# Optimization experiments

Measured on AMD Instinct MI355X. Metric: run time of the kernel, lower is better.

The kernel has to match this reference:

```python
import jax, jax.numpy as jnp
import numpy as np

B, T, C = 4, 2048, 2048
H, HKV = 16, 4
D = C // H            # 128
G = H // HKV          # 4 query heads per kv head
ROPE_THETA = 10000.0


def _rope_tables(seq_len, head_dim, theta):
    inv = 1.0 / (theta ** (np.arange(0, head_dim, 2, dtype=np.float32) / head_dim))
    t = np.arange(seq_len, dtype=np.float32)
    f = np.outer(t, inv)  # (T, D/2)
    return jnp.asarray(np.cos(f)), jnp.asarray(np.sin(f))


def setup_inputs() -> dict:
    key = jax.random.key(0)
    ks = jax.random.split(key, 5)
    x = jax.random.normal(ks[0], (B, T, C), dtype=jnp.float32)
    W_q = jax.random.normal(ks[1], (H * D, C), dtype=jnp.float32) * 0.02
    W_k = jax.random.normal(ks[2], (HKV * D, C), dtype=jnp.float32) * 0.02
    W_v = jax.random.normal(ks[3], (HKV * D, C), dtype=jnp.float32) * 0.02
    W_o = jax.random.normal(ks[4], (C, C), dtype=jnp.float32) * 0.02
    cos, sin = _rope_tables(T, D, ROPE_THETA)
    return {"x": x, "W_q": W_q, "W_k": W_k, "W_v": W_v, "W_o": W_o,
            "cos": cos, "sin": sin}


def _apply_rope(xh, cos, sin):
    # xh: (B, h, T, D); cos/sin: (T, D/2)
    x0 = xh[..., 0::2]
    x1 = xh[..., 1::2]
    c = cos[None, None, :, :]
    s = sin[None, None, :, :]
    o0 = x0 * c - x1 * s
    o1 = x0 * s + x1 * c
    return jnp.stack([o0, o1], axis=-1).reshape(xh.shape)


def reference(x, W_q, W_k, W_v, W_o, cos, sin):
    b, t, c = x.shape
    q = (x @ W_q.T).reshape(b, t, H, D).transpose(0, 2, 1, 3)      # (B,H,T,D)
    k = (x @ W_k.T).reshape(b, t, HKV, D).transpose(0, 2, 1, 3)    # (B,HKV,T,D)
    v = (x @ W_v.T).reshape(b, t, HKV, D).transpose(0, 2, 1, 3)
    q = _apply_rope(q, cos[:t], sin[:t])
    k = _apply_rope(k, cos[:t], sin[:t])
    # GQA via reshape instead of repeat_interleave (same head ordering:
    # q head index h = kv*G + g).
    qg = q.reshape(b, HKV, G, t, D)
    scores = jnp.einsum('bkgtd,bksd->bkgts', qg, k) / jnp.sqrt(jnp.float32(D))
    causal = jnp.tril(jnp.ones((t, t), dtype=bool))
    scores = jnp.where(causal[None, None, None, :, :], scores, -jnp.inf)
    attn = jax.nn.softmax(scores, axis=-1)
    out = jnp.einsum('bkgts,bksd->bkgtd', attn, v)                 # (B,HKV,G,T,D)
    out = out.reshape(b, H, t, D).transpose(0, 2, 1, 3).reshape(b, t, c)
    return out @ W_o.T
```

## Files before the change

### kernel.cpp

```cpp
#include <hip/hip_runtime.h>
#include <cmath>

typedef __attribute__((ext_vector_type(8))) short bf16x8;
typedef __attribute__((ext_vector_type(4))) float f32x4;
typedef unsigned short u16;

__device__ __forceinline__ u16 f2bf(float f) {
  union { float f; unsigned u; } x; x.f = f;
  return (u16)((x.u + 0x7FFFu + ((x.u >> 16) & 1u)) >> 16);
}

__device__ __forceinline__ void gload_lds16(const void* g, void* l) {
  __builtin_amdgcn_global_load_lds((const __attribute__((address_space(1))) unsigned*)g,
                                   (__attribute__((address_space(3))) unsigned*)l,
                                   16, 0, 0);
}

__global__ __launch_bounds__(256) void cast_bf16_kernel(const float* __restrict__ in,
                                                        u16* __restrict__ out, long n) {
  long i = (long)blockIdx.x * blockDim.x + threadIdx.x;
  long stride = (long)gridDim.x * blockDim.x;
  for (long j = i * 4; j < n; j += stride * 4) {
    float4 v = *(const float4*)(in + j);
    ushort4 o;
    o.x = f2bf(v.x); o.y = f2bf(v.y); o.z = f2bf(v.z); o.w = f2bf(v.w);
    *(ushort4*)(out + j) = o;
  }
}

template <int EPI>
__global__ __launch_bounds__(512, 2) void gemm_bt256(const u16* __restrict__ A,
                                                     const u16* __restrict__ B,
                                                     void* __restrict__ outp,
                                                     int M, int N, int K,
                                                     const float* __restrict__ cosp,
                                                     const float* __restrict__ sinp,
                                                     float scale) {
  __shared__ u16 lds[65536];
  const int tid = threadIdx.x;
  const int lane = tid & 63;
  const int l16 = lane & 15, lhi = lane >> 4;
  const int w = tid >> 6;
  const int wr = w >> 2, wc = w & 3;
  const int m0 = blockIdx.y * 256;
  const int n0 = blockIdx.x * 256;

  f32x4 acc[8][4];
#pragma unroll
  for (int i = 0; i < 8; ++i)
#pragma unroll
    for (int j = 0; j < 4; ++j) acc[i][j] = (f32x4)0.0f;

  const int NT = K >> 6;

  auto stage = [&](int t, int buf) {
    const int k0 = t << 6;
    u16* Ad = lds + buf * 32768;
    u16* Bd = Ad + 16384;
#pragma unroll
    for (int j = 0; j < 4; ++j) {
      int c = tid + j * 512;
      int row = c >> 3;
      int sboff = ((c & 7) * 16) ^ ((row & 7) << 4);
      gload_lds16(A + (size_t)(m0 + row) * K + k0 + (sboff >> 1), Ad + (size_t)c * 8);
    }
#pragma unroll
    for (int j = 0; j < 4; ++j) {
      int c = tid + j * 512;
      int row = c >> 3;
      int sboff = ((c & 7) * 16) ^ ((row & 7) << 4);
      gload_lds16(B + (size_t)(n0 + row) * K + k0 + (sboff >> 1), Bd + (size_t)c * 8);
    }
  };

  stage(0, 0);
  stage(1, 1);

  for (int t = 0; t < NT; ++t) {
    const int cur = t & 1;
    if (t + 1 < NT) { asm volatile("s_waitcnt vmcnt(8)" ::: "memory"); }
    else            { asm volatile("s_waitcnt vmcnt(0)" ::: "memory"); }
    __builtin_amdgcn_s_barrier();
    const char* Ab = (const char*)(lds + cur * 32768);
    const char* Bb = (const char*)(lds + cur * 32768 + 16384);
#pragma unroll
    for (int qm = 0; qm < 2; ++qm)
#pragma unroll
      for (int qn = 0; qn < 2; ++qn) {
        bf16x8 af[4][2], bfr[2][2];
#pragma unroll
        for (int mi = 0; mi < 4; ++mi) {
          int ra = wr * 128 + qm * 64 + mi * 16 + l16;
#pragma unroll
          for (int kk = 0; kk < 2; ++kk)
            af[mi][kk] = *(const bf16x8*)(Ab + ra * 128 + ((kk * 64 + lhi * 16) ^ ((ra & 7) << 4)));
        }
#pragma unroll
        for (int ni = 0; ni < 2; ++ni) {
          int rb = wc * 64 + qn * 32 + ni * 16 + l16;
#pragma unroll
          for (int kk = 0; kk < 2; ++kk)
            bfr[ni][kk] = *(const bf16x8*)(Bb + rb * 128 + ((kk * 64 + lhi * 16) ^ ((rb & 7) << 4)));
        }
        __builtin_amdgcn_s_setprio(1);
#pragma unroll
        for (int kk = 0; kk < 2; ++kk)
#pragma unroll
          for (int mi = 0; mi < 4; ++mi)
#pragma unroll
            for (int ni = 0; ni < 2; ++ni)
              acc[qm * 4 + mi][qn * 2 + ni] = __builtin_amdgcn_mfma_f32_16x16x32_bf16(
                  af[mi][kk], bfr[ni][kk], acc[qm * 4 + mi][qn * 2 + ni], 0, 0, 0);
        __builtin_amdgcn_s_setprio(0);
      }
    asm volatile("s_waitcnt lgkmcnt(0)" ::: "memory");
    __builtin_amdgcn_s_barrier();
    if (t + 2 < NT) stage(t + 2, cur);
  }

  if (EPI == 2) {
    float* o = (float*)outp;
#pragma unroll
    for (int mi8 = 0; mi8 < 8; ++mi8)
#pragma unroll
      for (int r = 0; r < 4; ++r) {
        int row = m0 + wr * 128 + mi8 * 16 + lhi * 4 + r;
#pragma unroll
        for (int nj = 0; nj < 4; ++nj) {
          int col = n0 + wc * 64 + nj * 16 + l16;
          o[(size_t)row * N + col] = acc[mi8][nj][r];
        }
      }
  } else {
    u16* o = (u16*)outp;
    const int nheads = N >> 7;
#pragma unroll
    for (int mi8 = 0; mi8 < 8; ++mi8)
#pragma unroll
      for (int r = 0; r < 4; ++r) {
        int row = m0 + wr * 128 + mi8 * 16 + lhi * 4 + r;
        int b = row >> 11;
        int tt = row & 2047;
#pragma unroll
        for (int nj = 0; nj < 4; ++nj) {
          int col = n0 + wc * 64 + nj * 16 + l16;
          int hh = col >> 7, dd = col & 127;
          float v = acc[mi8][nj][r];
          float p = __shfl_xor(v, 1);
          float c = cosp[tt * 64 + (dd >> 1)];
          float s = sinp[tt * 64 + (dd >> 1)];
          v = (lane & 1) ? fmaf(p, s, v * c) : fmaf(v, c, -p * s);
          v *= scale;
          o[((size_t)(b * nheads + hh) * 2048 + tt) * 128 + dd] = f2bf(v);
        }
      }
  }
}

template <int EPI>
__global__ __launch_bounds__(256) void gemm_bt(const u16* __restrict__ A,
                                               const u16* __restrict__ B,
                                               void* __restrict__ outp,
                                               u16* __restrict__ vtp,
                                               int M, int N, int K,
                                               const float* __restrict__ cosp,
                                               const float* __restrict__ sinp,
                                               float scale) {
  __shared__ u16 As[128 * 64];
  __shared__ u16 Bs[128 * 64];
  const int tid = threadIdx.x;
  const int lane = tid & 63;
  const int l16 = lane & 15, lhi = lane >> 4;
  const int w = tid >> 6;
  const int wr = w >> 1, wc = w & 1;
  const int m0 = blockIdx.y * 128;
  const int n0 = blockIdx.x * 128;
  const int wbase = tid - lane;

  f32x4 acc[4][4];
#pragma unroll
  for (int i = 0; i < 4; ++i)
#pragma unroll
    for (int j = 0; j < 4; ++j) acc[i][j] = (f32x4)0.0f;

  for (int k0 = 0; k0 < K; k0 += 64) {
    __syncthreads();
#pragma unroll
    for (int j = 0; j < 4; ++j) {
      int c = tid + j * 256;
      gload_lds16(A + (size_t)(m0 + (c >> 3)) * K + k0 + (c & 7) * 8,
                  As + (size_t)(wbase + j * 256) * 8);
    }
#pragma unroll
    for (int j = 0; j < 4; ++j) {
      int c = tid + j * 256;
      gload_lds16(B + (size_t)(n0 + (c >> 3)) * K + k0 + (c & 7) * 8,
                  Bs + (size_t)(wbase + j * 256) * 8);
    }
    __syncthreads();
#pragma unroll
    for (int kk = 0; kk < 64; kk += 32) {
      bf16x8 af[4], bfr[4];
#pragma unroll
      for (int mi = 0; mi < 4; ++mi)
        af[mi] = *(const bf16x8*)&As[(wr * 64 + mi * 16 + l16) * 64 + kk + lhi * 8];
#pragma unroll
      for (int ni = 0; ni < 4; ++ni)
        bfr[ni] = *(const bf16x8*)&Bs[(wc * 64 + ni * 16 + l16) * 64 + kk + lhi * 8];
#pragma unroll
      for (int mi = 0; mi < 4; ++mi)
#pragma unroll
        for (int ni = 0; ni < 4; ++ni)
          acc[mi][ni] = __builtin_amdgcn_mfma_f32_16x16x32_bf16(af[mi], bfr[ni], acc[mi][ni], 0, 0, 0);
    }
  }

  {
    const int bx = blockIdx.x;
    if (bx < 4) {
      u16* o = (u16*)outp;
#pragma unroll
      for (int mi = 0; mi < 4; ++mi)
#pragma unroll
        for (int r = 0; r < 4; ++r) {
          int row = m0 + wr * 64 + mi * 16 + lhi * 4 + r;
          int b = row >> 11;
          int t = row & 2047;
          size_t base = ((size_t)(b * 4 + bx) * 2048 + t) * 128;
#pragma unroll
          for (int ni = 0; ni < 4; ++ni) {
            int d = wc * 64 + ni * 16 + l16;
            float v = acc[mi][ni][r];
            float p = __shfl_xor(v, 1);
            float c = cosp[t * 64 + (d >> 1)];
            float s = sinp[t * 64 + (d >> 1)];
            v = (lane & 1) ? fmaf(p, s, v * c) : fmaf(v, c, -p * s);
            o[base + d] = f2bf(v);
          }
        }
    } else {
      const int kvh = bx - 4;
#pragma unroll
      for (int mi = 0; mi < 4; ++mi)
#pragma unroll
        for (int r = 0; r < 4; ++r) {
          int row = m0 + wr * 64 + mi * 16 + lhi * 4 + r;
          int b = row >> 11;
          int t = row & 2047;
          size_t base = ((size_t)(b * 4 + kvh) * 128) * 2048 + t;
#pragma unroll
          for (int ni = 0; ni < 4; ++ni) {
            int d = wc * 64 + ni * 16 + l16;
            vtp[base + (size_t)d * 2048] = f2bf(acc[mi][ni][r]);
          }
        }
    }
  }
}

__global__ __launch_bounds__(512, 4) void attn_kernel(const u16* __restrict__ Q,
                                                      const u16* __restrict__ Kp,
                                                      const u16* __restrict__ Vtp,
                                                      u16* __restrict__ O) {
  __shared__ u16 lds[25600];
  u16* Ks  = lds;
  u16* VTs = lds + 8192;
  u16* Pb  = lds + 16384;

  const int tid = threadIdx.x;
  const int lane = tid & 63;
  const int w = tid >> 6;
  const int l16 = lane & 15, lhi = lane >> 4;
  const int bid = blockIdx.x;
  const int qt = 15 - (bid >> 6);
  const int hb = bid & 63;
  const int h = hb >> 2;
  const int b = hb & 3;
  const int kvh = h >> 2;
  const int q0 = qt * 128;
  const int wbase = tid - lane;
  const int wrow0 = q0 + w * 16;

  const u16* Qb = Q + ((size_t)((b * 16 + h) * 2048 + wrow0)) * 128;
  const u16* Kb = Kp + (size_t)(b * 4 + kvh) * 2048 * 128;
  const u16* Vtb = Vtp + (size_t)(b * 4 + kvh) * 128 * 2048;

  u16* PP = Pb + w * 1152;

  bf16x8 qf[4];
#pragma unroll
  for (int ks = 0; ks < 4; ++ks)
    qf[ks] = *(const bf16x8*)(Qb + (size_t)l16 * 128 + ks * 32 + lhi * 8);

  f32x4 oacc[8];
#pragma unroll
  for (int i = 0; i < 8; ++i) oacc[i] = (f32x4)0.0f;
  float mrow[4], lrow[4];
#pragma unroll
  for (int r = 0; r < 4; ++r) { mrow[r] = -3.0e38f; lrow[r] = 0.0f; }

  const int nkt = 2 * qt + 2;
  for (int kt = 0; kt < nkt; ++kt) {
    const int t0 = kt * 64;
    __syncthreads();
#pragma unroll
    for (int j = 0; j < 2; ++j) {
      int c = tid + j * 512;
      int row = c >> 4;
      int sboff = ((c & 15) * 16) ^ ((row & 7) << 4);
      gload_lds16(Kb + (size_t)(t0 + row) * 128 + (sboff >> 1),
                  Ks + (size_t)(wbase + j * 512) * 8);
    }
#pragma unroll
    for (int j = 0; j < 2; ++j) {
      int c = tid + j * 512;
      int d = c >> 3;
      int sboff = ((c & 7) * 16) ^ ((d & 7) << 4);
      gload_lds16(Vtb + (size_t)d * 2048 + t0 + (sboff >> 1),
                  VTs + (size_t)(wbase + j * 512) * 8);
    }
    __syncthreads();

    if (t0 <= wrow0 + 15) {
      f32x4 sacc[4];
#pragma unroll
      for (int ni = 0; ni < 4; ++ni) sacc[ni] = (f32x4)0.0f;
      const char* ksb = (const char*)Ks;
#pragma unroll
      for (int ks = 0; ks < 4; ++ks)
#pragma unroll
        for (int ni = 0; ni < 4; ++ni) {
          int row = ni * 16 + l16;
          int boff = row * 256 + ((ks * 64 + lhi * 16) ^ ((l16 & 7) << 4));
          bf16x8 kf = *(const bf16x8*)(ksb + boff);
          sacc[ni] = __builtin_amdgcn_mfma_f32_16x16x32_bf16(qf[ks], kf, sacc[ni], 0, 0, 0);
        }

      if (t0 + 63 > wrow0) {
#pragma unroll
        for (int ni = 0; ni < 4; ++ni)
#pragma unroll
          for (int r = 0; r < 4; ++r) {
            int qrow = wrow0 + lhi * 4 + r;
            int kcol = t0 + ni * 16 + l16;
            if (kcol > qrow) sacc[ni][r] = -3.0e38f;
          }
      }

      float mnew[4];
      bool defer = true;
#pragma unroll
      for (int r = 0; r < 4; ++r) {
        float rm = fmaxf(fmaxf(sacc[0][r], sacc[1][r]), fmaxf(sacc[2][r], sacc[3][r]));
        rm = fmaxf(rm, __shfl_xor(rm, 1));
        rm = fmaxf(rm, __shfl_xor(rm, 2));
        rm = fmaxf(rm, __shfl_xor(rm, 4));
        rm = fmaxf(rm, __shfl_xor(rm, 8));
        mnew[r] = fmaxf(mrow[r], rm);
        defer = defer && (rm <= mrow[r] + 8.0f);
      }
      defer = __all(defer);
      if (defer) {
#pragma unroll
        for (int r = 0; r < 4; ++r) mnew[r] = mrow[r];
      } else {
#pragma unroll
        for (int r = 0; r < 4; ++r) {
          float sc = exp2f(mrow[r] - mnew[r]);
          mrow[r] = mnew[r];
          lrow[r] *= sc;
#pragma unroll
          for (int i = 0; i < 8; ++i) oacc[i][r] *= sc;
        }
      }
      float rs[4] = {0.f, 0.f, 0.f, 0.f};
#pragma unroll
      for (int ni = 0; ni < 4; ++ni)
#pragma unroll
        for (int r = 0; r < 4; ++r) {
          float p = exp2f(sacc[ni][r] - mnew[r]);
          rs[r] += p;
          PP[(lhi * 4 + r) * 72 + ni * 16 + l16] = f2bf(p);
        }
#pragma unroll
      for (int r = 0; r < 4; ++r) {
        float s2 = rs[r];
        s2 += __shfl_xor(s2, 1);
        s2 += __shfl_xor(s2, 2);
        s2 += __shfl_xor(s2, 4);
        s2 += __shfl_xor(s2, 8);
        lrow[r] += s2;
      }

      const char* vtb = (const char*)VTs;
#pragma unroll
      for (int ks = 0; ks < 2; ++ks) {
        bf16x8 pa = *(const bf16x8*)&PP[l16 * 72 + ks * 32 + lhi * 8];
#pragma unroll
        for (int nf = 0; nf < 8; ++nf) {
          int row = nf * 16 + l16;
          int boff = row * 128 + ((ks * 64 + lhi * 16) ^ ((l16 & 7) << 4));
          bf16x8 vb = *(const bf16x8*)(vtb + boff);
          oacc[nf] = __builtin_amdgcn_mfma_f32_16x16x32_bf16(pa, vb, oacc[nf], 0, 0, 0);
        }
      }
    }
  }

  float inv[4];
#pragma unroll
  for (int r = 0; r < 4; ++r) inv[r] = 1.0f / lrow[r];
  __syncthreads();
  u16* OS = lds + w * 2048;
#pragma unroll
  for (int nf = 0; nf < 8; ++nf)
#pragma unroll
    for (int r = 0; r < 4; ++r)
      OS[(lhi * 4 + r) * 128 + nf * 16 + l16] = f2bf(oacc[nf][r] * inv[r]);
  __syncthreads();
  u16* Ob = O + ((size_t)(b * 2048 + wrow0)) * 2048 + h * 128;
#pragma unroll
  for (int j = 0; j < 4; ++j) {
    int c = lane + j * 64;
    int row = c >> 4, dc = (c & 15) * 8;
    *(bf16x8*)(Ob + (size_t)row * 2048 + dc) = *(const bf16x8*)&OS[row * 128 + dc];
  }
}

extern "C" void kernel_launch(void* const* d_in, const int* in_sizes, int n_in,
                              void* d_out, int out_size, void* d_ws, size_t ws_size,
                              hipStream_t stream) {
  (void)in_sizes; (void)n_in; (void)out_size; (void)ws_size;
  const float* x    = (const float*)d_in[0];
  const float* Wq   = (const float*)d_in[1];
  const float* Wk   = (const float*)d_in[2];
  const float* Wv   = (const float*)d_in[3];
  const float* Wo   = (const float*)d_in[4];
  const float* cosp = (const float*)d_in[5];
  const float* sinp = (const float*)d_in[6];

  u16* ws  = (u16*)d_ws;
  u16* xbf = ws;
  u16* Wqb = xbf + 16777216;
  u16* Wkb = Wqb + 4194304;
  u16* Wvb = Wkb + 1048576;
  u16* Wob = Wvb + 1048576;
  u16* Qb  = Wob + 4194304;
  u16* Kb  = Qb + 16777216;
  u16* Vb  = Kb + 4194304;
  u16* AO  = xbf;

  cast_bf16_kernel<<<2048, 256, 0, stream>>>(x,  xbf, 16777216L);
  cast_bf16_kernel<<<512,  256, 0, stream>>>(Wq, Wqb, 4194304L);
  cast_bf16_kernel<<<256,  256, 0, stream>>>(Wk, Wkb, 1048576L);
  cast_bf16_kernel<<<256,  256, 0, stream>>>(Wv, Wvb, 1048576L);
  cast_bf16_kernel<<<512,  256, 0, stream>>>(Wo, Wob, 4194304L);

  const float qscale = (float)(1.4426950408889634 / sqrt(128.0));

  gemm_bt256<0><<<dim3(8, 32), 512, 0, stream>>>(xbf, Wqb, Qb, 8192, 2048, 2048, cosp, sinp, qscale);
  gemm_bt<3><<<dim3(8, 64), 256, 0, stream>>>(xbf, Wkb, Kb, Vb, 8192, 1024, 2048, cosp, sinp, 1.0f);

  attn_kernel<<<1024, 512, 0, stream>>>(Qb, Kb, Vb, AO);

  gemm_bt256<2><<<dim3(8, 32), 512, 0, stream>>>(AO, Wob, d_out, 8192, 2048, 2048, nullptr, nullptr, 1.0f);
}
```

Baseline: 391.0 us.

## Rewrite attention with 32x32 MFMA, transposed scores and register-resident P

The attention kernel switches from 16x16x32 to 32x32x16 bf16 MFMA. It computes S^T (K times Q) so each lane owns a single query row, and the row max and sum shrink to one cross-half shuffle instead of four. P is packed to bf16 with v_cvt_pk_bf16_f32 and exchanged between lanes rather than going through an LDS scratch buffer, which removes the P buffer and its LDS traffic. Blocks drop to 256 threads with 4 waves of 32 query rows each, which changes occupancy and doubles the per-thread K/V load count and register pressure.

```diff
diff --git a/kernel.cpp b/kernel.cpp
--- a/kernel.cpp
+++ b/kernel.cpp
@@ -3,11 +3,18 @@
 
 typedef __attribute__((ext_vector_type(8))) short bf16x8;
 typedef __attribute__((ext_vector_type(4))) float f32x4;
+typedef __attribute__((ext_vector_type(16))) float f32x16;
 typedef unsigned short u16;
 
 __device__ __forceinline__ u16 f2bf(float f) {
   union { float f; unsigned u; } x; x.f = f;
   return (u16)((x.u + 0x7FFFu + ((x.u >> 16) & 1u)) >> 16);
+}
+
+__device__ __forceinline__ unsigned cvtpk(float lo, float hi) {
+  unsigned r;
+  asm("v_cvt_pk_bf16_f32 %0, %1, %2" : "=v"(r) : "v"(lo), "v"(hi));
+  return r;
 }
 
 __device__ __forceinline__ void gload_lds16(const void* g, void* l) {
@@ -258,19 +265,18 @@
   }
 }
 
-__global__ __launch_bounds__(512, 4) void attn_kernel(const u16* __restrict__ Q,
+__global__ __launch_bounds__(256, 2) void attn_kernel(const u16* __restrict__ Q,
                                                       const u16* __restrict__ Kp,
                                                       const u16* __restrict__ Vtp,
                                                       u16* __restrict__ O) {
-  __shared__ u16 lds[25600];
+  __shared__ u16 lds[17408];
   u16* Ks  = lds;
   u16* VTs = lds + 8192;
-  u16* Pb  = lds + 16384;
 
   const int tid = threadIdx.x;
   const int lane = tid & 63;
   const int w = tid >> 6;
-  const int l16 = lane & 15, lhi = lane >> 4;
+  const int l5 = lane & 31, hi = lane >> 5;
   const int bid = blockIdx.x;
   const int qt = 15 - (bid >> 6);
   const int hb = bid & 63;
@@ -279,151 +285,155 @@
   const int kvh = h >> 2;
   const int q0 = qt * 128;
   const int wbase = tid - lane;
-  const int wrow0 = q0 + w * 16;
+  const int wrow0 = q0 + w * 32;
+  const int qg = wrow0 + l5;
 
   const u16* Qb = Q + ((size_t)((b * 16 + h) * 2048 + wrow0)) * 128;
   const u16* Kb = Kp + (size_t)(b * 4 + kvh) * 2048 * 128;
   const u16* Vtb = Vtp + (size_t)(b * 4 + kvh) * 128 * 2048;
 
-  u16* PP = Pb + w * 1152;
-
-  bf16x8 qf[4];
-#pragma unroll
-  for (int ks = 0; ks < 4; ++ks)
-    qf[ks] = *(const bf16x8*)(Qb + (size_t)l16 * 128 + ks * 32 + lhi * 8);
-
-  f32x4 oacc[8];
-#pragma unroll
-  for (int i = 0; i < 8; ++i) oacc[i] = (f32x4)0.0f;
-  float mrow[4], lrow[4];
-#pragma unroll
-  for (int r = 0; r < 4; ++r) { mrow[r] = -3.0e38f; lrow[r] = 0.0f; }
+  bf16x8 qf[8];
+#pragma unroll
+  for (int ks = 0; ks < 8; ++ks)
+    qf[ks] = *(const bf16x8*)(Qb + (size_t)l5 * 128 + ks * 16 + hi * 8);
+
+  f32x16 oacc[4];
+#pragma unroll
+  for (int i = 0; i < 4; ++i) oacc[i] = (f32x16)0.0f;
+  float m = -3.0e38f, l = 0.0f;
 
   const int nkt = 2 * qt + 2;
   for (int kt = 0; kt < nkt; ++kt) {
     const int t0 = kt * 64;
     __syncthreads();
 #pragma unroll
-    for (int j = 0; j < 2; ++j) {
-      int c = tid + j * 512;
+    for (int j = 0; j < 4; ++j) {
+      int c = tid + j * 256;
       int row = c >> 4;
-      int sboff = ((c & 15) * 16) ^ ((row & 7) << 4);
+      int sboff = ((c & 15) * 16) ^ ((row & 15) << 4);
       gload_lds16(Kb + (size_t)(t0 + row) * 128 + (sboff >> 1),
-                  Ks + (size_t)(wbase + j * 512) * 8);
-    }
-#pragma unroll
-    for (int j = 0; j < 2; ++j) {
-      int c = tid + j * 512;
+                  Ks + (size_t)(wbase + j * 256) * 8);
+    }
+#pragma unroll
+    for (int j = 0; j < 4; ++j) {
+      int c = tid + j * 256;
       int d = c >> 3;
       int sboff = ((c & 7) * 16) ^ ((d & 7) << 4);
       gload_lds16(Vtb + (size_t)d * 2048 + t0 + (sboff >> 1),
-                  VTs + (size_t)(wbase + j * 512) * 8);
+                  VTs + (size_t)(wbase + j * 256) * 8);
     }
     __syncthreads();
 
-    if (t0 <= wrow0 + 15) {
-      f32x4 sacc[4];
-#pragma unroll
-      for (int ni = 0; ni < 4; ++ni) sacc[ni] = (f32x4)0.0f;
+    if (t0 <= wrow0 + 31) {
+      float p[32];
       const char* ksb = (const char*)Ks;
 #pragma unroll
-      for (int ks = 0; ks < 4; ++ks)
-#pragma unroll
-        for (int ni = 0; ni < 4; ++ni) {
-          int row = ni * 16 + l16;
-          int boff = row * 256 + ((ks * 64 + lhi * 16) ^ ((l16 & 7) << 4));
-          bf16x8 kf = *(const bf16x8*)(ksb + boff);
-          sacc[ni] = __builtin_amdgcn_mfma_f32_16x16x32_bf16(qf[ks], kf, sacc[ni], 0, 0, 0);
-        }
+      for (int kt2 = 0; kt2 < 2; ++kt2) {
+        f32x16 sacc = (f32x16)0.0f;
+        int row = kt2 * 32 + l5;
+#pragma unroll
+        for (int ks = 0; ks < 8; ++ks) {
+          bf16x8 kf = *(const bf16x8*)(ksb + row * 256 + ((ks * 32 + hi * 16) ^ ((row & 15) << 4)));
+          sacc = __builtin_amdgcn_mfma_f32_32x32x16_bf16(kf, qf[ks], sacc, 0, 0, 0);
+        }
+#pragma unroll
+        for (int r = 0; r < 16; ++r) p[kt2 * 16 + r] = sacc[r];
+      }
 
       if (t0 + 63 > wrow0) {
 #pragma unroll
-        for (int ni = 0; ni < 4; ++ni)
-#pragma unroll
-          for (int r = 0; r < 4; ++r) {
-            int qrow = wrow0 + lhi * 4 + r;
-            int kcol = t0 + ni * 16 + l16;
-            if (kcol > qrow) sacc[ni][r] = -3.0e38f;
+        for (int kt2 = 0; kt2 < 2; ++kt2)
+#pragma unroll
+          for (int r = 0; r < 16; ++r) {
+            int kvg = t0 + kt2 * 32 + (r & 3) + 8 * (r >> 2) + 4 * hi;
+            if (kvg > qg) p[kt2 * 16 + r] = -3.0e38f;
           }
       }
 
-      float mnew[4];
-      bool defer = true;
-#pragma unroll
-      for (int r = 0; r < 4; ++r) {
-        float rm = fmaxf(fmaxf(sacc[0][r], sacc[1][r]), fmaxf(sacc[2][r], sacc[3][r]));
-        rm = fmaxf(rm, __shfl_xor(rm, 1));
-        rm = fmaxf(rm, __shfl_xor(rm, 2));
-        rm = fmaxf(rm, __shfl_xor(rm, 4));
-        rm = fmaxf(rm, __shfl_xor(rm, 8));
-        mnew[r] = fmaxf(mrow[r], rm);
-        defer = defer && (rm <= mrow[r] + 8.0f);
-      }
-      defer = __all(defer);
-      if (defer) {
-#pragma unroll
-        for (int r = 0; r < 4; ++r) mnew[r] = mrow[r];
-      } else {
-#pragma unroll
-        for (int r = 0; r < 4; ++r) {
-          float sc = exp2f(mrow[r] - mnew[r]);
-          mrow[r] = mnew[r];
-          lrow[r] *= sc;
-#pragma unroll
-          for (int i = 0; i < 8; ++i) oacc[i][r] *= sc;
-        }
-      }
-      float rs[4] = {0.f, 0.f, 0.f, 0.f};
-#pragma unroll
-      for (int ni = 0; ni < 4; ++ni)
-#pragma unroll
-        for (int r = 0; r < 4; ++r) {
-          float p = exp2f(sacc[ni][r] - mnew[r]);
-          rs[r] += p;
-          PP[(lhi * 4 + r) * 72 + ni * 16 + l16] = f2bf(p);
-        }
-#pragma unroll
-      for (int r = 0; r < 4; ++r) {
-        float s2 = rs[r];
-        s2 += __shfl_xor(s2, 1);
-        s2 += __shfl_xor(s2, 2);
-        s2 += __shfl_xor(s2, 4);
-        s2 += __shfl_xor(s2, 8);
-        lrow[r] += s2;
-      }
+      float mx[16];
+#pragma unroll
+      for (int i = 0; i < 16; ++i) mx[i] = fmaxf(p[i], p[i + 16]);
+#pragma unroll
+      for (int i = 0; i < 8; ++i) mx[i] = fmaxf(mx[i], mx[i + 8]);
+#pragma unroll
+      for (int i = 0; i < 4; ++i) mx[i] = fmaxf(mx[i], mx[i + 4]);
+      float rm = fmaxf(fmaxf(mx[0], mx[1]), fmaxf(mx[2], mx[3]));
+      rm = fmaxf(rm, __shfl_xor(rm, 32));
+
+      bool defer = __all(rm <= m + 8.0f);
+      if (!defer) {
+        float mnew = fmaxf(m, rm);
+        float sc = exp2f(m - mnew);
+        m = mnew;
+        l *= sc;
+#pragma unroll
+        for (int i = 0; i < 4; ++i)
+#pragma unroll
+          for (int r = 0; r < 16; ++r) oacc[i][r] *= sc;
+      }
+
+#pragma unroll
+      for (int i = 0; i < 32; ++i) p[i] = exp2f(p[i] - m);
+      float sm[16];
+#pragma unroll
+      for (int i = 0; i < 16; ++i) sm[i] = p[i] + p[i + 16];
+#pragma unroll
+      for (int i = 0; i < 8; ++i) sm[i] += sm[i + 8];
+#pragma unroll
+      for (int i = 0; i < 4; ++i) sm[i] += sm[i + 4];
+      float s2 = (sm[0] + sm[1]) + (sm[2] + sm[3]);
+      s2 += __shfl_xor(s2, 32);
+      l += s2;
 
       const char* vtb = (const char*)VTs;
 #pragma unroll
-      for (int ks = 0; ks < 2; ++ks) {
-        bf16x8 pa = *(const bf16x8*)&PP[l16 * 72 + ks * 32 + lhi * 8];
-#pragma unroll
-        for (int nf = 0; nf < 8; ++nf) {
-          int row = nf * 16 + l16;
-          int boff = row * 128 + ((ks * 64 + lhi * 16) ^ ((l16 & 7) << 4));
-          bf16x8 vb = *(const bf16x8*)(vtb + boff);
-          oacc[nf] = __builtin_amdgcn_mfma_f32_16x16x32_bf16(pa, vb, oacc[nf], 0, 0, 0);
-        }
-      }
-    }
-  }
-
-  float inv[4];
-#pragma unroll
-  for (int r = 0; r < 4; ++r) inv[r] = 1.0f / lrow[r];
+      for (int kt2 = 0; kt2 < 2; ++kt2) {
+#pragma unroll
+        for (int sl = 0; sl < 2; ++sl) {
+          int base = kt2 * 16 + sl * 8;
+          unsigned A0 = cvtpk(p[base + 0], p[base + 1]);
+          unsigned A1 = cvtpk(p[base + 2], p[base + 3]);
+          unsigned A2 = cvtpk(p[base + 4], p[base + 5]);
+          unsigned A3 = cvtpk(p[base + 6], p[base + 7]);
+          unsigned XA0 = __shfl_xor(A0, 32);
+          unsigned XA1 = __shfl_xor(A1, 32);
+          unsigned XA2 = __shfl_xor(A2, 32);
+          unsigned XA3 = __shfl_xor(A3, 32);
+          union { unsigned u[4]; bf16x8 v; } pf;
+          pf.u[0] = hi ? XA2 : A0;
+          pf.u[1] = hi ? XA3 : A1;
+          pf.u[2] = hi ? A2 : XA0;
+          pf.u[3] = hi ? A3 : XA1;
+          int s = kt2 * 2 + sl;
+#pragma unroll
+          for (int dt = 0; dt < 4; ++dt) {
+            int row = dt * 32 + l5;
+            bf16x8 vb = *(const bf16x8*)(vtb + row * 128 + ((s * 32 + hi * 16) ^ ((row & 7) << 4)));
+            oacc[dt] = __builtin_amdgcn_mfma_f32_32x32x16_bf16(vb, pf.v, oacc[dt], 0, 0, 0);
+          }
+        }
+      }
+    }
+  }
+
+  float inv = 1.0f / l;
   __syncthreads();
-  u16* OS = lds + w * 2048;
-#pragma unroll
-  for (int nf = 0; nf < 8; ++nf)
-#pragma unroll
-    for (int r = 0; r < 4; ++r)
-      OS[(lhi * 4 + r) * 128 + nf * 16 + l16] = f2bf(oacc[nf][r] * inv[r]);
+  u16* OS = lds + w * 4352;
+#pragma unroll
+  for (int dt = 0; dt < 4; ++dt)
+#pragma unroll
+    for (int r = 0; r < 16; ++r) {
+      int d = dt * 32 + (r & 3) + 8 * (r >> 2) + 4 * hi;
+      OS[l5 * 136 + d] = f2bf(oacc[dt][r] * inv);
+    }
   __syncthreads();
-  u16* Ob = O + ((size_t)(b * 2048 + wrow0)) * 2048 + h * 128;
-#pragma unroll
-  for (int j = 0; j < 4; ++j) {
-    int c = lane + j * 64;
-    int row = c >> 4, dc = (c & 15) * 8;
-    *(bf16x8*)(Ob + (size_t)row * 2048 + dc) = *(const bf16x8*)&OS[row * 128 + dc];
+  u16* Ob = O + ((size_t)(b * 2048 + q0)) * 2048 + h * 128;
+#pragma unroll
+  for (int j = 0; j < 8; ++j) {
+    int c = tid + j * 256;
+    int row = c >> 4, col = c & 15;
+    *(bf16x8*)(Ob + (size_t)row * 2048 + col * 8) =
+        *(const bf16x8*)&lds[(row >> 5) * 4352 + (row & 31) * 136 + col * 8];
   }
 }
 
@@ -461,7 +471,7 @@
   gemm_bt256<0><<<dim3(8, 32), 512, 0, stream>>>(xbf, Wqb, Qb, 8192, 2048, 2048, cosp, sinp, qscale);
   gemm_bt<3><<<dim3(8, 64), 256, 0, stream>>>(xbf, Wkb, Kb, Vb, 8192, 1024, 2048, cosp, sinp, 1.0f);
 
-  attn_kernel<<<1024, 512, 0, stream>>>(Qb, Kb, Vb, AO);
+  attn_kernel<<<1024, 256, 0, stream>>>(Qb, Kb, Vb, AO);
 
   gemm_bt256<2><<<dim3(8, 32), 512, 0, stream>>>(AO, Wob, d_out, 8192, 2048, 2048, nullptr, nullptr, 1.0f);
 }
```

Result: faster. 338.7 us (-13.4%).
